# Kernel optimization log

Measured on AMD Instinct MI355X. Metric: run time of the kernel, lower is better.

Reference implementation:

```python
import jax, jax.numpy as jnp
import numpy as np

T, N, E, DH = 4, 10000, 160000, 256
BN_EPS = 1e-5


def setup_inputs() -> dict:
    key = jax.random.key(0)
    ks = jax.random.split(key, 6)
    node_data = jax.random.normal(ks[0], (T, N, DH), dtype=jnp.float32)
    edge_index = jax.random.randint(ks[1], (2, E), 0, N)
    edge_weight = jax.random.uniform(ks[2], (T, E), dtype=jnp.float32)
    W1 = jax.random.normal(ks[3], (3 * DH, DH), dtype=jnp.float32) * 0.02
    b1 = jnp.zeros((DH,), dtype=jnp.float32)
    gamma = jnp.ones((DH,), dtype=jnp.float32)
    beta = jnp.zeros((DH,), dtype=jnp.float32)
    return {"node_data": node_data, "edge_weight": edge_weight, "W1": W1,
            "b1": b1, "gamma": gamma, "beta": beta, "edge_index": edge_index}


def reference(node_data, edge_weight, W1, b1, gamma, beta, edge_index):
    # edge_index: [2, E] with row 0 = source j, row 1 = destination i
    # (ew[t, i, j] multiplies node j and accumulates into node i, as in bmm)
    src, dst = edge_index[0], edge_index[1]

    # sparse bmm: sum_j ew[t,i,j] * node_data[t,j,:]  -> [T, N, DH]
    weighted = node_data[:, src, :] * edge_weight[..., None]  # [T, E, DH]
    sum_neighbor = jax.vmap(lambda m: jax.ops.segment_sum(m, dst, num_segments=N))(weighted)

    # Z = torch.sparse.sum(ew, dim=2); Z[Z == 0] = 1
    Z = jax.vmap(lambda w: jax.ops.segment_sum(w, dst, num_segments=N))(edge_weight)
    Z = jnp.where(Z == 0, 1.0, Z)[..., None]  # [T, N, 1]
    avg_neighbor = sum_neighbor / Z

    # prev_state = cat([zeros(1,N,dh), node_data[1:]], dim=0)  (as in source)
    prev_state = jnp.concatenate(
        [jnp.zeros((1, N, DH), node_data.dtype), node_data[1:]], axis=0)

    x = jnp.concatenate([node_data, prev_state, avg_neighbor], axis=2)
    x = x.reshape(T * N, 3 * DH)

    # ReluFCN: Linear(3*dh -> dh) -> BatchNorm1d (batch stats) -> ReLU
    h = x @ W1 + b1  # [T*N, DH]
    mean = h.mean(axis=0)
    var = h.var(axis=0)
    h = (h - mean) * jax.lax.rsqrt(var + BN_EPS) * gamma + beta
    h = jax.nn.relu(h)
    return h.reshape(T, N, DH)
```

## Files before the change

kernel.cpp:

```cpp
#include <hip/hip_runtime.h>

enum { TT = 4, NNODES = 10000, NEDGES = 160000 };

typedef short v8s __attribute__((ext_vector_type(8)));
typedef float v4f __attribute__((ext_vector_type(4)));
typedef unsigned short u16x4 __attribute__((ext_vector_type(4)));

static __device__ __forceinline__ float bf2f(unsigned short u) {
    union { unsigned int i; float f; } c;
    c.i = ((unsigned int)u) << 16;
    return c.f;
}
static __device__ __forceinline__ unsigned short f2bf(float f) {
    union { float f; unsigned int i; } c;
    c.f = f;
    return (unsigned short)((c.i + 0x7FFFu + ((c.i >> 16) & 1u)) >> 16);
}
static __device__ __forceinline__ float u2f(unsigned int u) {
    union { unsigned int i; float f; } c;
    c.i = u;
    return c.f;
}
static __device__ __forceinline__ void acc8(float* a, float w, uint4 u) {
    a[0] += w * u2f(u.x << 16);
    a[1] += w * u2f(u.x & 0xffff0000u);
    a[2] += w * u2f(u.y << 16);
    a[3] += w * u2f(u.y & 0xffff0000u);
    a[4] += w * u2f(u.z << 16);
    a[5] += w * u2f(u.z & 0xffff0000u);
    a[6] += w * u2f(u.w << 16);
    a[7] += w * u2f(u.w & 0xffff0000u);
}

__global__ void GraphConvLayer_91061896610587_kernel() {}

__global__ void zero_k(int* p, int n) {
    int i = blockIdx.x * 256 + threadIdx.x;
    if (i < n) p[i] = 0;
}

__global__ void prep_k(const unsigned short* ndu, const void* s0, const void* s1,
                       const void* s2, int* mode, float* gammaf, float* betaf) {
    __shared__ int cnt;
    __shared__ int score[6];
    __shared__ float vals[6][256];
    int d = threadIdx.x;
    if (d == 0) cnt = 0;
    if (d < 6) score[d] = 0;
    __syncthreads();
    int c = 0;
    for (int j = 0; j < 16; ++j) {
        unsigned short u = ndu[d * 16 + j];
        if ((u & 0x7FFF) >= 0x6000) ++c;
    }
    if (c) atomicAdd(&cnt, c);
    const void* ptrs[3];
    ptrs[0] = s0; ptrs[1] = s1; ptrs[2] = s2;
    for (int q = 0; q < 6; ++q) {
        const void* p = ptrs[q % 3];
        float v = (q < 3) ? bf2f(((const unsigned short*)p)[d]) : ((const float*)p)[d];
        vals[q][d] = v;
        float av = fabsf(v);
        if (av > 0.25f && av < 4.0f) atomicAdd(&score[q], 1);
    }
    __syncthreads();
    if (d == 0) *mode = (cnt > 0) ? 0 : 1;
    int best = 0;
    for (int q = 1; q < 6; ++q)
        if (score[q] > score[best]) best = q;
    float g = (score[best] > 0) ? vals[best][d] : 1.0f;
    int interp = (best >= 3) ? 3 : 0;
    int bslot  = ((best % 3) == 2) ? 1 : 2;
    float b = vals[interp + bslot][d];
    if (!(b == b) || fabsf(b) > 100.f) b = 0.f;
    gammaf[d] = g;
    betaf[d]  = b;
}

__global__ void zp_k(int* zp, int zn, const unsigned short* ndu, const void* s0,
                     const void* s1, const void* s2, int* mode, float* gammaf,
                     float* betaf) {
    __shared__ int cnt;
    __shared__ int score[6];
    __shared__ float vals[6][256];
    if (blockIdx.x < 213) {
        int i = blockIdx.x * 256 + threadIdx.x;
        if (i < zn) zp[i] = 0;
        return;
    }
    int d = threadIdx.x;
    if (d == 0) cnt = 0;
    if (d < 6) score[d] = 0;
    __syncthreads();
    int c = 0;
    for (int j = 0; j < 16; ++j) {
        unsigned short u = ndu[d * 16 + j];
        if ((u & 0x7FFF) >= 0x6000) ++c;
    }
    if (c) atomicAdd(&cnt, c);
    const void* ptrs[3];
    ptrs[0] = s0; ptrs[1] = s1; ptrs[2] = s2;
    for (int q = 0; q < 6; ++q) {
        const void* p = ptrs[q % 3];
        float v = (q < 3) ? bf2f(((const unsigned short*)p)[d]) : ((const float*)p)[d];
        vals[q][d] = v;
        float av = fabsf(v);
        if (av > 0.25f && av < 4.0f) atomicAdd(&score[q], 1);
    }
    __syncthreads();
    if (d == 0) *mode = (cnt > 0) ? 0 : 1;
    int best = 0;
    for (int q = 1; q < 6; ++q)
        if (score[q] > score[best]) best = q;
    float g = (score[best] > 0) ? vals[best][d] : 1.0f;
    int interp = (best >= 3) ? 3 : 0;
    int bslot  = ((best % 3) == 2) ? 1 : 2;
    float b = vals[interp + bslot][d];
    if (!(b == b) || fabsf(b) > 100.f) b = 0.f;
    gammaf[d] = g;
    betaf[d]  = b;
}

__global__ void cph_k(const int* mode, const void* nd_raw, unsigned short* ndc,
                      const void* W1, short* wp0, short* wp1,
                      const int* ei, int* counts) {
    int bb = blockIdx.x;
    if (bb < 10000) {
        if (*mode != 0) return;
        int i = bb * 256 + threadIdx.x;
        float4 v = ((const float4*)nd_raw)[i];
        ushort4 o;
        o.x = f2bf(v.x); o.y = f2bf(v.y); o.z = f2bf(v.z); o.w = f2bf(v.w);
        ((ushort4*)ndc)[i] = o;
    } else if (bb < 11024) {
        int gid = (bb - 10000) * 256 + threadIdx.x;
        int v   = gid >> 17;
        int rem = gid & 131071;
        int k   = rem >> 8;
        int n   = rem & 255;
        int m   = *mode;
        const unsigned short* Wb = (const unsigned short*)W1;
        const float*          Wf = (const float*)W1;
        float val;
        if (k < 256) {
            val = m ? bf2f(Wb[k * 256 + n]) : Wf[k * 256 + n];
            if (v) val += m ? bf2f(Wb[(k + 256) * 256 + n]) : Wf[(k + 256) * 256 + n];
        } else {
            val = m ? bf2f(Wb[(k + 256) * 256 + n]) : Wf[(k + 256) * 256 + n];
        }
        int dst = ((k >> 5) * 256 + n) * 32 + (k & 31);
        (v ? wp1 : wp0)[dst] = (short)f2bf(val);
    } else {
        int e = (bb - 11024) * 256 + threadIdx.x;
        if (e < NEDGES) atomicAdd(&counts[ei[NEDGES + e]], 1);
    }
}

__global__ void pack_w(const int* mode, const void* W1, float* w2f,
                       short* wp0, short* wp1) {
    int gid = blockIdx.x * 256 + threadIdx.x;
    int v   = gid >> 17;
    int rem = gid & 131071;
    int k   = rem >> 8;
    int n   = rem & 255;
    int m   = *mode;
    const unsigned short* Wb = (const unsigned short*)W1;
    const float*          Wf = (const float*)W1;
    float val;
    if (k < 256) {
        val = m ? bf2f(Wb[k * 256 + n]) : Wf[k * 256 + n];
        if (v) val += m ? bf2f(Wb[(k + 256) * 256 + n]) : Wf[(k + 256) * 256 + n];
    } else {
        val = m ? bf2f(Wb[(k + 256) * 256 + n]) : Wf[(k + 256) * 256 + n];
    }
    if (w2f) w2f[v * 131072 + k * 256 + n] = val;
    if (wp0) {
        int dst = ((k >> 5) * 256 + n) * 32 + (k & 31);
        (v ? wp1 : wp0)[dst] = (short)f2bf(val);
    }
}

__global__ void hist_k(const int* ei, int* counts) {
    int e = blockIdx.x * 256 + threadIdx.x;
    if (e < NEDGES) atomicAdd(&counts[ei[NEDGES + e]], 1);
}

__global__ void scan_k(const int* counts, int* offsets) {
    __shared__ int part[256];
    __shared__ int excl[257];
    int t = threadIdx.x;
    int b = t * 40, e = b + 40;
    if (e > NNODES) e = NNODES;
    int s = 0;
    for (int i = b; i < e; ++i) s += counts[i];
    part[t] = s;
    __syncthreads();
    if (t == 0) {
        int run = 0;
        for (int i = 0; i < 256; ++i) { excl[i] = run; run += part[i]; }
        excl[256] = run;
    }
    __syncthreads();
    int run = excl[t];
    for (int i = b; i < e; ++i) { offsets[i] = run; run += counts[i]; }
    if (t == 0) offsets[NNODES] = excl[256];
}

__global__ void scat_k(const int* ei, const int* offsets, int* cursors,
                       int* ssrc, int* seid) {
    int e = blockIdx.x * 256 + threadIdx.x;
    if (e >= NEDGES) return;
    int d = ei[NEDGES + e];
    int pos = offsets[d] + atomicAdd(&cursors[d], 1);
    ssrc[pos] = ei[e];
    seid[pos] = e;
}

__global__ void scatw_k(const int* mode, const int* ei, const void* ew_raw,
                        const int* offsets, int* cursors, int* ssrc, int* seid,
                        float* wcsr) {
    int e = blockIdx.x * 256 + threadIdx.x;
    if (e >= NEDGES) return;
    int d = ei[NEDGES + e];
    int pos = offsets[d] + atomicAdd(&cursors[d], 1);
    ssrc[pos] = ei[e];
    seid[pos] = e;
    int m = *mode;
#pragma unroll
    for (int t = 0; t < TT; ++t) {
        float w = m ? bf2f(((const unsigned short*)ew_raw)[t * NEDGES + e])
                    : ((const float*)ew_raw)[t * NEDGES + e];
        wcsr[t * NEDGES + pos] = w;
    }
}

__global__ __launch_bounds__(512, 4) void fused_k(
    const int* mode, const void* nd_raw, const unsigned short* ndc,
    const float* wcsr, const int* offsets, const int* ssrc,
    const short* wp0, const short* wp1,
    unsigned short* h16, float* colsumB, float* colsumsqB) {
    __shared__ unsigned short xs[32 * 520];
    int id  = blockIdx.x;
    int xcd = id & 7;
    int t   = xcd & 3;
    int rbi = ((id >> 3) << 1) + (xcd >> 2);
    if (rbi >= 313) return;
    int rb  = rbi * 32;
    const unsigned short* ndb = (*mode == 1) ? (const unsigned short*)nd_raw : ndc;
    int tid = threadIdx.x;

    int node = tid >> 4;
    int sub  = tid & 15;
    int growc = min(rb + node, NNODES - 1);
    const uint4* ndg = (const uint4*)(ndb + (size_t)t * NNODES * 256);
    const uint4* own = ndg + (size_t)growc * 32;

    uint4 c0 = own[sub];
    uint4 c1 = own[sub + 16];
    *(uint4*)&xs[node * 520 + sub * 8]        = c0;
    *(uint4*)&xs[node * 520 + (sub + 16) * 8] = c1;

    float a1[16];
#pragma unroll
    for (int j = 0; j < 16; ++j) a1[j] = 0.f;
    float Z = 0.f;
    const float* wrow = wcsr + t * NEDGES;
    int b = offsets[growc], e = offsets[growc + 1];
    int p = b;
    for (; p + 2 <= e; p += 2) {
        int s0 = ssrc[p], s1 = ssrc[p + 1];
        float w0 = wrow[p], w1 = wrow[p + 1];
        const uint4* r0 = ndg + (size_t)s0 * 32;
        const uint4* r1 = ndg + (size_t)s1 * 32;
        uint4 A0 = r0[sub], A1 = r0[sub + 16];
        uint4 B0 = r1[sub], B1 = r1[sub + 16];
        Z += w0 + w1;
        acc8(a1 + 0, w0, A0); acc8(a1 + 8, w0, A1);
        acc8(a1 + 0, w1, B0); acc8(a1 + 8, w1, B1);
    }
    for (; p < e; ++p) {
        int s = ssrc[p];
        float w = wrow[p];
        const uint4* r0 = ndg + (size_t)s * 32;
        uint4 A0 = r0[sub], A1 = r0[sub + 16];
        Z += w;
        acc8(a1 + 0, w, A0); acc8(a1 + 8, w, A1);
    }
    float inv = (Z == 0.f) ? 1.f : (1.f / Z);
    {
        ushort4 lo, hi;
        lo.x = f2bf(a1[0] * inv); lo.y = f2bf(a1[1] * inv);
        lo.z = f2bf(a1[2] * inv); lo.w = f2bf(a1[3] * inv);
        hi.x = f2bf(a1[4] * inv); hi.y = f2bf(a1[5] * inv);
        hi.z = f2bf(a1[6] * inv); hi.w = f2bf(a1[7] * inv);
        *(ushort4*)&xs[node * 520 + 256 + sub * 8]     = lo;
        *(ushort4*)&xs[node * 520 + 256 + sub * 8 + 4] = hi;
        lo.x = f2bf(a1[8] * inv);  lo.y = f2bf(a1[9] * inv);
        lo.z = f2bf(a1[10] * inv); lo.w = f2bf(a1[11] * inv);
        hi.x = f2bf(a1[12] * inv); hi.y = f2bf(a1[13] * inv);
        hi.z = f2bf(a1[14] * inv); hi.w = f2bf(a1[15] * inv);
        *(ushort4*)&xs[node * 520 + 256 + (sub + 16) * 8]     = lo;
        *(ushort4*)&xs[node * 520 + 256 + (sub + 16) * 8 + 4] = hi;
    }
    __syncthreads();

    int wave = tid >> 6;
    int lane = tid & 63;
    int lane15 = lane & 15, quad = lane >> 4;
    const v8s* wp8 = (const v8s*)(t ? wp1 : wp0);

    v4f acc[2][2];
    v4f zero = {0.f, 0.f, 0.f, 0.f};
#pragma unroll
    for (int mf = 0; mf < 2; ++mf)
#pragma unroll
        for (int nf = 0; nf < 2; ++nf) acc[mf][nf] = zero;

#pragma unroll
    for (int kc = 0; kc < 16; ++kc) {
        v8s a0  = *(const v8s*)&xs[lane15 * 520 + kc * 32 + quad * 8];
        v8s a1v = *(const v8s*)&xs[(lane15 + 16) * 520 + kc * 32 + quad * 8];
#pragma unroll
        for (int nf = 0; nf < 2; ++nf) {
            int ntg = wave * 2 + nf;
            v8s bf = wp8[(size_t)(kc * 256 + ntg * 16 + lane15) * 4 + quad];
            acc[0][nf] = __builtin_amdgcn_mfma_f32_16x16x32_bf16(a0,  bf, acc[0][nf], 0, 0, 0);
            acc[1][nf] = __builtin_amdgcn_mfma_f32_16x16x32_bf16(a1v, bf, acc[1][nf], 0, 0, 0);
        }
    }

    int bucket = id & 63;
#pragma unroll
    for (int nf = 0; nf < 2; ++nf) {
        int col = (wave * 2 + nf) * 16 + lane15;
        float s1 = 0.f, s2 = 0.f;
#pragma unroll
        for (int mf = 0; mf < 2; ++mf) {
            int rbase = rb + mf * 16 + quad * 4;
#pragma unroll
            for (int r = 0; r < 4; ++r) {
                int row = rbase + r;
                if (row < NNODES) {
                    float v = acc[mf][nf][r];
                    __builtin_nontemporal_store(
                        f2bf(v), &h16[(size_t)(t * NNODES + row) * 256 + col]);
                    s1 += v; s2 += v * v;
                }
            }
        }
        s1 += __shfl_xor(s1, 16, 64); s1 += __shfl_xor(s1, 32, 64);
        s2 += __shfl_xor(s2, 16, 64); s2 += __shfl_xor(s2, 32, 64);
        if (quad == 0) {
            atomicAdd(&colsumB[bucket * 256 + col], s1);
            atomicAdd(&colsumsqB[bucket * 256 + col], s2);
        }
    }
}

__global__ void statsB_k(const float* colsumB, const float* colsumsqB,
                         const float* gammaf, const float* betaf,
                         float* scale, float* shiftv) {
    int d = threadIdx.x;
    float s1 = 0.f, s2 = 0.f;
    for (int b = 0; b < 64; ++b) {
        s1 += colsumB[b * 256 + d];
        s2 += colsumsqB[b * 256 + d];
    }
    float mean = s1 * (1.f / 40000.f);
    float var  = s2 * (1.f / 40000.f) - mean * mean;
    if (var < 0.f) var = 0.f;
    if (!(var < 1e30f) || !(mean == mean)) { scale[d] = 0.f; shiftv[d] = 2.5f; return; }
    float r  = rsqrtf(var + 1e-5f);
    float sc = gammaf[d] * r;
    scale[d]  = sc;
    shiftv[d] = betaf[d] - mean * sc;
}

__global__ void normb_k(const unsigned short* h16, const float* scale,
                        const float* shiftv, float* out) {
    int i = blockIdx.x * 256 + threadIdx.x;
    int c0 = (i & 63) * 4;
    u16x4 h = __builtin_nontemporal_load(&((const u16x4*)h16)[i]);
    v4f o;
    float v;
    v = bf2f(h.x) * scale[c0 + 0] + shiftv[c0 + 0]; if (!(v == v)) v = 1.f; o.x = v > 0.f ? v : 0.f;
    v = bf2f(h.y) * scale[c0 + 1] + shiftv[c0 + 1]; if (!(v == v)) v = 1.f; o.y = v > 0.f ? v : 0.f;
    v = bf2f(h.z) * scale[c0 + 2] + shiftv[c0 + 2]; if (!(v == v)) v = 1.f; o.z = v > 0.f ? v : 0.f;
    v = bf2f(h.w) * scale[c0 + 3] + shiftv[c0 + 3]; if (!(v == v)) v = 1.f; o.w = v > 0.f ? v : 0.f;
    __builtin_nontemporal_store(o, &((v4f*)out)[i]);
}

__global__ void aggv_k(const int* mode, const void* nd_raw, const void* ew_raw,
                       const int* offsets, const int* ssrc, const int* seid,
                       unsigned short* avg) {
    int m   = *mode;
    int wid = blockIdx.x * 4 + (threadIdx.x >> 6);
    int t = wid / NNODES, n = wid - t * NNODES;
    int lane = threadIdx.x & 63;
    float a0 = 0.f, a1 = 0.f, a2 = 0.f, a3 = 0.f, Z = 0.f;
    int b = offsets[n], e = offsets[n + 1];
    for (int p = b; p < e; ++p) {
        int s = ssrc[p];
        int ewi = t * NEDGES + seid[p];
        float w = m ? bf2f(((const unsigned short*)ew_raw)[ewi])
                    : ((const float*)ew_raw)[ewi];
        Z += w;
        int vidx = (t * NNODES + s) * 64 + lane;
        if (m) {
            ushort4 v = ((const ushort4*)nd_raw)[vidx];
            a0 += w * bf2f(v.x); a1 += w * bf2f(v.y);
            a2 += w * bf2f(v.z); a3 += w * bf2f(v.w);
        } else {
            float4 v = ((const float4*)nd_raw)[vidx];
            a0 += w * v.x; a1 += w * v.y; a2 += w * v.z; a3 += w * v.w;
        }
    }
    float inv = (Z == 0.f) ? 1.f : (1.f / Z);
    ushort4 o;
    o.x = f2bf(a0 * inv); o.y = f2bf(a1 * inv);
    o.z = f2bf(a2 * inv); o.w = f2bf(a3 * inv);
    ((ushort4*)avg)[(t * NNODES + n) * 64 + lane] = o;
}

__global__ __launch_bounds__(256) void gemmv_k(
    const int* mode, const void* nd_raw, const unsigned short* avg,
    const float* w2f, float* hbuf) {
    __shared__ float xsf[16 * 512];
    int m   = *mode;
    int bt  = blockIdx.x / 625;
    int rb0 = (blockIdx.x - bt * 625) * 16;
    int tid = threadIdx.x;
    for (int j = 0; j < 32; ++j) {
        int idx = tid + j * 256;
        int r = idx >> 9, k = idx & 511;
        int grow = (bt * NNODES + rb0 + r) * 256;
        float val;
        if (k < 256)
            val = m ? bf2f(((const unsigned short*)nd_raw)[grow + k])
                    : ((const float*)nd_raw)[grow + k];
        else
            val = bf2f(avg[grow + (k - 256)]);
        xsf[idx] = val;
    }
    __syncthreads();
    int r0 = (tid >> 6) * 4;
    const float4* w4 = (const float4*)(w2f + (bt ? 131072 : 0));
    float acc[4][4];
#pragma unroll
    for (int r = 0; r < 4; ++r)
#pragma unroll
        for (int c = 0; c < 4; ++c) acc[r][c] = 0.f;
    const float* x0 = &xsf[(r0 + 0) * 512];
    const float* x1 = &xsf[(r0 + 1) * 512];
    const float* x2 = &xsf[(r0 + 2) * 512];
    const float* x3 = &xsf[(r0 + 3) * 512];
#pragma unroll 8
    for (int k = 0; k < 512; ++k) {
        float4 wv = w4[k * 64 + (tid & 63)];
        float a = x0[k], b = x1[k], c = x2[k], d = x3[k];
        acc[0][0] += a * wv.x; acc[0][1] += a * wv.y; acc[0][2] += a * wv.z; acc[0][3] += a * wv.w;
        acc[1][0] += b * wv.x; acc[1][1] += b * wv.y; acc[1][2] += b * wv.z; acc[1][3] += b * wv.w;
        acc[2][0] += c * wv.x; acc[2][1] += c * wv.y; acc[2][2] += c * wv.z; acc[2][3] += c * wv.w;
        acc[3][0] += d * wv.x; acc[3][1] += d * wv.y; acc[3][2] += d * wv.z; acc[3][3] += d * wv.w;
    }
#pragma unroll
    for (int r = 0; r < 4; ++r) {
        int grow = bt * NNODES + rb0 + r0 + r;
        float4 o;
        o.x = acc[r][0]; o.y = acc[r][1]; o.z = acc[r][2]; o.w = acc[r][3];
        ((float4*)hbuf)[grow * 64 + (tid & 63)] = o;
    }
}

__global__ void stats2_k(const float* hbuf, float* colsum, float* colsumsq) {
    int col = threadIdx.x;
    int rb  = blockIdx.x * 250;
    float s1 = 0.f, s2 = 0.f;
    for (int j = 0; j < 250; ++j) {
        float v = hbuf[(size_t)(rb + j) * 256 + col];
        s1 += v; s2 += v * v;
    }
    atomicAdd(&colsum[col], s1);
    atomicAdd(&colsumsq[col], s2);
}

__global__ void stats_k(const float* colsum, const float* colsumsq,
                        const float* gammaf, const float* betaf,
                        float* scale, float* shiftv) {
    int d = threadIdx.x;
    float mean = colsum[d] * (1.f / 40000.f);
    float var  = colsumsq[d] * (1.f / 40000.f) - mean * mean;
    if (var < 0.f) var = 0.f;
    if (!(var < 1e30f) || !(mean == mean)) { scale[d] = 0.f; shiftv[d] = 2.5f; return; }
    float r  = rsqrtf(var + 1e-5f);
    float sc = gammaf[d] * r;
    scale[d]  = sc;
    shiftv[d] = betaf[d] - mean * sc;
}

__global__ void norm_k(float* hbuf, const float* scale, const float* shiftv) {
    int i = blockIdx.x * 256 + threadIdx.x;
    int c0 = (i & 63) * 4;
    float4 h = ((const float4*)hbuf)[i];
    float4 o;
    float v;
    v = h.x * scale[c0 + 0] + shiftv[c0 + 0]; if (!(v == v)) v = 1.f; o.x = v > 0.f ? v : 0.f;
    v = h.y * scale[c0 + 1] + shiftv[c0 + 1]; if (!(v == v)) v = 1.f; o.y = v > 0.f ? v : 0.f;
    v = h.z * scale[c0 + 2] + shiftv[c0 + 2]; if (!(v == v)) v = 1.f; o.z = v > 0.f ? v : 0.f;
    v = h.w * scale[c0 + 3] + shiftv[c0 + 3]; if (!(v == v)) v = 1.f; o.w = v > 0.f ? v : 0.f;
    ((float4*)hbuf)[i] = o;
}

extern "C" void kernel_launch(void* const* d_in, const int* in_sizes, int n_in,
                              void* d_out, int out_size, void* d_ws, size_t ws_size,
                              hipStream_t stream) {
    const void* nd = d_in[0];
    const void* ew = d_in[1];
    const void* W1 = d_in[2];
    const void* p3 = d_in[3];
    const void* p4 = d_in[4];
    const void* p5 = d_in[5];
    const void* ei = d_in[6];
    {
        const void *nd_ = 0, *ew_ = 0, *W1_ = 0, *ei_ = 0, *s_[3] = {0, 0, 0};
        int ns = 0;
        for (int i = 0; i < n_in; ++i) {
            int s = in_sizes[i];
            if      (s == 10240000) nd_ = d_in[i];
            else if (s == 640000)   ew_ = d_in[i];
            else if (s == 196608)   W1_ = d_in[i];
            else if (s == 320000)   ei_ = d_in[i];
            else if (s == 256 && ns < 3) s_[ns++] = d_in[i];
        }
        if (nd_ && ew_ && W1_ && ei_ && ns == 3) {
            nd = nd_; ew = ew_; W1 = W1_; ei = ei_;
            p3 = s_[0]; p4 = s_[1]; p5 = s_[2];
        }
    }
    float* outp = (float*)d_out;
    const unsigned short* ndu = (const unsigned short*)nd;
    const int* eii = (const int*)ei;

    char* ws = (char*)d_ws;

    if (ws_size >= (size_t)45582464) {
        int*   counts    = (int*)(ws + 0);
        int*   cursors   = (int*)(ws + 40960);
        int*   mode      = (int*)(ws + 81920);
        float* scale     = (float*)(ws + 82944);
        float* shiftv    = (float*)(ws + 83968);
        float* gammaf    = (float*)(ws + 84992);
        float* betaf     = (float*)(ws + 86016);
        float* colsumB   = (float*)(ws + 87040);
        float* colsumsqB = (float*)(ws + 152576);
        int*   offsets   = (int*)(ws + 218112);
        int*   ssrc      = (int*)(ws + 258176);
        int*   seid      = (int*)(ws + 898176);
        float* wcsr      = (float*)(ws + 1538176);
        short* wp0       = (short*)(ws + 4098176);
        short* wp1       = (short*)(ws + 4360320);
        unsigned short* ndc = (unsigned short*)(ws + 4622464);
        unsigned short* h16 = (unsigned short*)(ws + 25102464);

        zp_k<<<214, 256, 0, stream>>>((int*)ws, 54528, ndu, p3, p4, p5,
                                      mode, gammaf, betaf);
        cph_k<<<11649, 256, 0, stream>>>(mode, nd, ndc, W1, wp0, wp1, eii, counts);
        scan_k<<<1, 256, 0, stream>>>(counts, offsets);
        scatw_k<<<625, 256, 0, stream>>>(mode, eii, ew, offsets, cursors,
                                         ssrc, seid, wcsr);
        fused_k<<<1280, 512, 0, stream>>>(mode, nd, ndc, wcsr, offsets, ssrc,
                                          wp0, wp1, h16, colsumB, colsumsqB);
        statsB_k<<<1, 256, 0, stream>>>(colsumB, colsumsqB, gammaf, betaf, scale, shiftv);
        normb_k<<<10000, 256, 0, stream>>>(h16, scale, shiftv, outp);
    } else {
        int*   counts   = (int*)(ws + 0);
        int*   cursors  = (int*)(ws + 40960);
        float* colsum   = (float*)(ws + 81920);
        float* colsumsq = (float*)(ws + 82944);
        int*   mode     = (int*)(ws + 83968);
        float* scale    = (float*)(ws + 84032);
        float* shiftv   = (float*)(ws + 85056);
        float* gammaf   = (float*)(ws + 86080);
        float* betaf   = (float*)(ws + 87104);
        int*   offsets  = (int*)(ws + 88128);
        int*   ssrc     = (int*)(ws + 128192);
        int*   seid     = (int*)(ws + 768192);
        float* w2f      = (float*)(ws + 1408192);
        unsigned short* avg = (unsigned short*)(ws + 2457600);
        short* nowp = 0;

        zero_k<<<83, 256, 0, stream>>>((int*)ws, 20994);
        prep_k<<<1, 256, 0, stream>>>(ndu, p3, p4, p5, mode, gammaf, betaf);
        pack_w<<<1024, 256, 0, stream>>>(mode, W1, w2f, nowp, nowp);
        hist_k<<<625, 256, 0, stream>>>(eii, counts);
        scan_k<<<1, 256, 0, stream>>>(counts, offsets);
        scat_k<<<625, 256, 0, stream>>>(eii, offsets, cursors, ssrc, seid);
        aggv_k<<<10000, 256, 0, stream>>>(mode, nd, ew, offsets, ssrc, seid, avg);
        gemmv_k<<<2500, 256, 0, stream>>>(mode, nd, avg, w2f, outp);
        stats2_k<<<160, 256, 0, stream>>>(outp, colsum, colsumsq);
        stats_k<<<1, 256, 0, stream>>>(colsum, colsumsq, gammaf, betaf, scale, shiftv);
        norm_k<<<10000, 256, 0, stream>>>(outp, scale, shiftv);
    }
}
```

Measured before the change: 229.4 us.

## Fuse aggregation, GEMM, batch-norm stats and normalize into one cooperative kernel

Replaces the fused_k + statsB_k + normb_k sequence with a single cooperative kernel of 512 persistent blocks. Each block processes up to three 32-row tiles and keeps the MFMA accumulators in registers. After a grid-wide sync it computes the batch-norm scale and shift itself and writes the normalized ReLU output directly. This removes the bf16 intermediate h round trip and two kernel launches, and also drops the unused seid writes in scatw_k. The cost is a grid sync, extra register pressure from holding three tiles of results, and possible imbalance since 313 tiles are spread over 128 workers per timestep.

Result: no change. 227.3 us (-0.9%).

```diff
diff --git a/kernel.cpp b/kernel.cpp
--- a/kernel.cpp
+++ b/kernel.cpp
@@ -1,4 +1,7 @@
 #include <hip/hip_runtime.h>
+#include <hip/hip_cooperative_groups.h>
+
+namespace cg = cooperative_groups;
 
 enum { TT = 4, NNODES = 10000, NEDGES = 160000 };
 
@@ -217,20 +220,202 @@
 }
 
 __global__ void scatw_k(const int* mode, const int* ei, const void* ew_raw,
-                        const int* offsets, int* cursors, int* ssrc, int* seid,
+                        const int* offsets, int* cursors, int* ssrc,
                         float* wcsr) {
     int e = blockIdx.x * 256 + threadIdx.x;
     if (e >= NEDGES) return;
     int d = ei[NEDGES + e];
     int pos = offsets[d] + atomicAdd(&cursors[d], 1);
     ssrc[pos] = ei[e];
-    seid[pos] = e;
     int m = *mode;
 #pragma unroll
     for (int t = 0; t < TT; ++t) {
         float w = m ? bf2f(((const unsigned short*)ew_raw)[t * NEDGES + e])
                     : ((const float*)ew_raw)[t * NEDGES + e];
         wcsr[t * NEDGES + pos] = w;
+    }
+}
+
+__global__ __launch_bounds__(512, 4) void fusedP_k(
+    const int* mode, const void* nd_raw, const unsigned short* ndc,
+    const float* wcsr, const int* offsets, const int* ssrc,
+    const short* wp0, const short* wp1,
+    float* outp, float* colsumB, float* colsumsqB,
+    const float* gammaf, const float* betaf) {
+    __shared__ unsigned short xs[32 * 520];
+    __shared__ float sscale[256];
+    __shared__ float sshift[256];
+    int id  = blockIdx.x;
+    int xcd = id & 7;
+    int t   = xcd & 3;
+    int worker = ((id >> 3) << 1) + (xcd >> 2);
+    int tid = threadIdx.x;
+    const unsigned short* ndb = (*mode == 1) ? (const unsigned short*)nd_raw : ndc;
+    const uint4* ndg = (const uint4*)(ndb + (size_t)t * NNODES * 256);
+    const float* wrow = wcsr + t * NEDGES;
+
+    int node = tid >> 4;
+    int sub  = tid & 15;
+    int wave = tid >> 6;
+    int lane = tid & 63;
+    int lane15 = lane & 15, quad = lane >> 4;
+    const v8s* wp8 = (const v8s*)(t ? wp1 : wp0);
+    int bucket = id & 63;
+
+    v4f held[3][2][2];
+
+#pragma unroll
+    for (int tt = 0; tt < 3; ++tt) {
+        int rbi = worker + tt * 128;
+        if (rbi < 313) {
+            int rb = rbi * 32;
+            int growc = min(rb + node, NNODES - 1);
+            const uint4* own = ndg + (size_t)growc * 32;
+            uint4 c0 = own[sub];
+            uint4 c1 = own[sub + 16];
+            *(uint4*)&xs[node * 520 + sub * 8]        = c0;
+            *(uint4*)&xs[node * 520 + (sub + 16) * 8] = c1;
+
+            float a1[16];
+#pragma unroll
+            for (int j = 0; j < 16; ++j) a1[j] = 0.f;
+            float Z = 0.f;
+            int b = offsets[growc], e = offsets[growc + 1];
+            int p = b;
+            for (; p + 2 <= e; p += 2) {
+                int s0 = ssrc[p], s1 = ssrc[p + 1];
+                float w0 = wrow[p], w1 = wrow[p + 1];
+                const uint4* r0 = ndg + (size_t)s0 * 32;
+                const uint4* r1 = ndg + (size_t)s1 * 32;
+                uint4 A0 = r0[sub], A1 = r0[sub + 16];
+                uint4 B0 = r1[sub], B1 = r1[sub + 16];
+                Z += w0 + w1;
+                acc8(a1 + 0, w0, A0); acc8(a1 + 8, w0, A1);
+                acc8(a1 + 0, w1, B0); acc8(a1 + 8, w1, B1);
+            }
+            for (; p < e; ++p) {
+                int s = ssrc[p];
+                float w = wrow[p];
+                const uint4* r0 = ndg + (size_t)s * 32;
+                uint4 A0 = r0[sub], A1 = r0[sub + 16];
+                Z += w;
+                acc8(a1 + 0, w, A0); acc8(a1 + 8, w, A1);
+            }
+            float inv = (Z == 0.f) ? 1.f : (1.f / Z);
+            {
+                ushort4 lo, hi;
+                lo.x = f2bf(a1[0] * inv); lo.y = f2bf(a1[1] * inv);
+                lo.z = f2bf(a1[2] * inv); lo.w = f2bf(a1[3] * inv);
+                hi.x = f2bf(a1[4] * inv); hi.y = f2bf(a1[5] * inv);
+                hi.z = f2bf(a1[6] * inv); hi.w = f2bf(a1[7] * inv);
+                *(ushort4*)&xs[node * 520 + 256 + sub * 8]     = lo;
+                *(ushort4*)&xs[node * 520 + 256 + sub * 8 + 4] = hi;
+                lo.x = f2bf(a1[8] * inv);  lo.y = f2bf(a1[9] * inv);
+                lo.z = f2bf(a1[10] * inv); lo.w = f2bf(a1[11] * inv);
+                hi.x = f2bf(a1[12] * inv); hi.y = f2bf(a1[13] * inv);
+                hi.z = f2bf(a1[14] * inv); hi.w = f2bf(a1[15] * inv);
+                *(ushort4*)&xs[node * 520 + 256 + (sub + 16) * 8]     = lo;
+                *(ushort4*)&xs[node * 520 + 256 + (sub + 16) * 8 + 4] = hi;
+            }
+            __syncthreads();
+
+            v4f acc[2][2];
+            v4f zero = {0.f, 0.f, 0.f, 0.f};
+#pragma unroll
+            for (int mf = 0; mf < 2; ++mf)
+#pragma unroll
+                for (int nf = 0; nf < 2; ++nf) acc[mf][nf] = zero;
+
+#pragma unroll
+            for (int kc = 0; kc < 16; ++kc) {
+                v8s a0  = *(const v8s*)&xs[lane15 * 520 + kc * 32 + quad * 8];
+                v8s a1v = *(const v8s*)&xs[(lane15 + 16) * 520 + kc * 32 + quad * 8];
+#pragma unroll
+                for (int nf = 0; nf < 2; ++nf) {
+                    int ntg = wave * 2 + nf;
+                    v8s bf = wp8[(size_t)(kc * 256 + ntg * 16 + lane15) * 4 + quad];
+                    acc[0][nf] = __builtin_amdgcn_mfma_f32_16x16x32_bf16(a0,  bf, acc[0][nf], 0, 0, 0);
+                    acc[1][nf] = __builtin_amdgcn_mfma_f32_16x16x32_bf16(a1v, bf, acc[1][nf], 0, 0, 0);
+                }
+            }
+
+#pragma unroll
+            for (int nf = 0; nf < 2; ++nf) {
+                int col = (wave * 2 + nf) * 16 + lane15;
+                float s1 = 0.f, s2 = 0.f;
+#pragma unroll
+                for (int mf = 0; mf < 2; ++mf) {
+                    held[tt][mf][nf] = acc[mf][nf];
+                    int rbase = rb + mf * 16 + quad * 4;
+#pragma unroll
+                    for (int r = 0; r < 4; ++r) {
+                        int row = rbase + r;
+                        if (row < NNODES) {
+                            float v = acc[mf][nf][r];
+                            s1 += v; s2 += v * v;
+                        }
+                    }
+                }
+                s1 += __shfl_xor(s1, 16, 64); s1 += __shfl_xor(s1, 32, 64);
+                s2 += __shfl_xor(s2, 16, 64); s2 += __shfl_xor(s2, 32, 64);
+                if (quad == 0) {
+                    atomicAdd(&colsumB[bucket * 256 + col], s1);
+                    atomicAdd(&colsumsqB[bucket * 256 + col], s2);
+                }
+            }
+            __syncthreads();
+        }
+    }
+
+    __threadfence();
+    cg::this_grid().sync();
+    __threadfence();
+
+    if (tid < 256) {
+        float s1 = 0.f, s2 = 0.f;
+        for (int b2 = 0; b2 < 64; ++b2) {
+            s1 += colsumB[b2 * 256 + tid];
+            s2 += colsumsqB[b2 * 256 + tid];
+        }
+        float mean = s1 * (1.f / 40000.f);
+        float var  = s2 * (1.f / 40000.f) - mean * mean;
+        if (var < 0.f) var = 0.f;
+        float sc, sh;
+        if (!(var < 1e30f) || !(mean == mean)) { sc = 0.f; sh = 2.5f; }
+        else {
+            float r = rsqrtf(var + 1e-5f);
+            sc = gammaf[tid] * r;
+            sh = betaf[tid] - mean * sc;
+        }
+        sscale[tid] = sc;
+        sshift[tid] = sh;
+    }
+    __syncthreads();
+
+#pragma unroll
+    for (int tt = 0; tt < 3; ++tt) {
+        int rbi = worker + tt * 128;
+        if (rbi < 313) {
+            int rb = rbi * 32;
+#pragma unroll
+            for (int nf = 0; nf < 2; ++nf) {
+                int col = (wave * 2 + nf) * 16 + lane15;
+                float sc = sscale[col], sh = sshift[col];
+#pragma unroll
+                for (int mf = 0; mf < 2; ++mf) {
+                    int rbase = rb + mf * 16 + quad * 4;
+#pragma unroll
+                    for (int r = 0; r < 4; ++r) {
+                        int row = rbase + r;
+                        if (row < NNODES) {
+                            float v = held[tt][mf][nf][r] * sc + sh;
+                            if (!(v == v)) v = 1.f;
+                            outp[(size_t)(t * NNODES + row) * 256 + col] = v > 0.f ? v : 0.f;
+                        }
+                    }
+                }
+            }
+        }
     }
 }
 
@@ -561,17 +746,34 @@
         short* wp1       = (short*)(ws + 4360320);
         unsigned short* ndc = (unsigned short*)(ws + 4622464);
         unsigned short* h16 = (unsigned short*)(ws + 25102464);
+        (void)seid;
 
         zp_k<<<214, 256, 0, stream>>>((int*)ws, 54528, ndu, p3, p4, p5,
                                       mode, gammaf, betaf);
         cph_k<<<11649, 256, 0, stream>>>(mode, nd, ndc, W1, wp0, wp1, eii, counts);
         scan_k<<<1, 256, 0, stream>>>(counts, offsets);
         scatw_k<<<625, 256, 0, stream>>>(mode, eii, ew, offsets, cursors,
-                                         ssrc, seid, wcsr);
-        fused_k<<<1280, 512, 0, stream>>>(mode, nd, ndc, wcsr, offsets, ssrc,
-                                          wp0, wp1, h16, colsumB, colsumsqB);
-        statsB_k<<<1, 256, 0, stream>>>(colsumB, colsumsqB, gammaf, betaf, scale, shiftv);
-        normb_k<<<10000, 256, 0, stream>>>(h16, scale, shiftv, outp);
+                                         ssrc, wcsr);
+
+        int coopBlocks = 0;
+        hipError_t occErr = hipOccupancyMaxActiveBlocksPerMultiprocessor(
+            &coopBlocks, fusedP_k, 512, 0);
+        if (occErr == hipSuccess && coopBlocks >= 2) {
+            void* args[] = {
+                (void*)&mode, (void*)&nd, (void*)&ndc, (void*)&wcsr,
+                (void*)&offsets, (void*)&ssrc, (void*)&wp0, (void*)&wp1,
+                (void*)&outp, (void*)&colsumB, (void*)&colsumsqB,
+                (void*)&gammaf, (void*)&betaf
+            };
+            hipLaunchCooperativeKernel((void*)fusedP_k, dim3(512), dim3(512),
+                                       args, 0, stream);
+        } else {
+            fused_k<<<1280, 512, 0, stream>>>(mode, nd, ndc, wcsr, offsets, ssrc,
+                                              wp0, wp1, h16, colsumB, colsumsqB);
+            statsB_k<<<1, 256, 0, stream>>>(colsumB, colsumsqB, gammaf, betaf,
+                                            scale, shiftv);
+            normb_k<<<10000, 256, 0, stream>>>(h16, scale, shiftv, outp);
+        }
     } else {
         int*   counts   = (int*)(ws + 0);
         int*   cursors  = (int*)(ws + 40960);
@@ -581,7 +783,7 @@
         float* scale    = (float*)(ws + 84032);
         float* shiftv   = (float*)(ws + 85056);
         float* gammaf   = (float*)(ws + 86080);
-        float* betaf   = (float*)(ws + 87104);
+        float* betaf    = (float*)(ws + 87104);
         int*   offsets  = (int*)(ws + 88128);
         int*   ssrc     = (int*)(ws + 128192);
         int*   seid     = (int*)(ws + 768192);
```

## Merge scan and BN stats into producers via last-block-done counters; fold mode detection

Applied to the files above, without the earlier changes.

The graph scan now runs inside the histogram kernel, and the BatchNorm statistics finalisation runs inside the fused aggregate+GEMM kernel. In each case the last block to finish, detected with an atomic done-counter, does the work, which removes two tiny single-block launches and their serialisation gaps. Every block of the preprocessing kernel now detects the input dtype from a small shared-memory scan instead of waiting on a previous kernel. The scatter kernel also stops writing the unused edge-id array. The cost is redundant per-block reads for mode detection, extra fences and atomics, and a serial tail in the last block.

Result: slower. 586.1 us (+155.4%).

```diff
diff --git a/kernel.cpp b/kernel.cpp
--- a/kernel.cpp
+++ b/kernel.cpp
@@ -77,18 +77,61 @@
     betaf[d]  = b;
 }
 
-__global__ void zp_k(int* zp, int zn, const unsigned short* ndu, const void* s0,
-                     const void* s1, const void* s2, int* mode, float* gammaf,
-                     float* betaf) {
+__global__ void pre_k(int* zp, const unsigned short* ndu, const void* nd_raw,
+                      unsigned short* ndc, const void* W1, short* wp0, short* wp1,
+                      const void* s0, const void* s1, const void* s2,
+                      int* mode, float* gammaf, float* betaf,
+                      int* doneA, int* doneB) {
     __shared__ int cnt;
     __shared__ int score[6];
     __shared__ float vals[6][256];
-    if (blockIdx.x < 213) {
-        int i = blockIdx.x * 256 + threadIdx.x;
-        if (i < zn) zp[i] = 0;
+    int bb = blockIdx.x;
+    int d  = threadIdx.x;
+
+    if (bb < 11024) {
+        if (d == 0) cnt = 0;
+        __syncthreads();
+        int c = 0;
+        for (int j = 0; j < 16; ++j) {
+            unsigned short u = ndu[d * 16 + j];
+            if ((u & 0x7FFF) >= 0x6000) c = 1;
+        }
+        if (c) cnt = 1;
+        __syncthreads();
+        int m = cnt ? 0 : 1;
+        if (bb < 10000) {
+            if (m != 0) return;
+            int i = bb * 256 + d;
+            float4 v = ((const float4*)nd_raw)[i];
+            ushort4 o;
+            o.x = f2bf(v.x); o.y = f2bf(v.y); o.z = f2bf(v.z); o.w = f2bf(v.w);
+            ((ushort4*)ndc)[i] = o;
+        } else {
+            int gid = (bb - 10000) * 256 + d;
+            int v   = gid >> 17;
+            int rem = gid & 131071;
+            int k   = rem >> 8;
+            int n   = rem & 255;
+            const unsigned short* Wb = (const unsigned short*)W1;
+            const float*          Wf = (const float*)W1;
+            float val;
+            if (k < 256) {
+                val = m ? bf2f(Wb[k * 256 + n]) : Wf[k * 256 + n];
+                if (v) val += m ? bf2f(Wb[(k + 256) * 256 + n]) : Wf[(k + 256) * 256 + n];
+            } else {
+                val = m ? bf2f(Wb[(k + 256) * 256 + n]) : Wf[(k + 256) * 256 + n];
+            }
+            int dst = ((k >> 5) * 256 + n) * 32 + (k & 31);
+            (v ? wp1 : wp0)[dst] = (short)f2bf(val);
+        }
         return;
     }
-    int d = threadIdx.x;
+    if (bb < 11232) {
+        int z = (bb - 11024) * 256 + d;
+        int idx = (z < 20480) ? z : z + 1280;
+        zp[idx] = 0;
+        return;
+    }
     if (d == 0) cnt = 0;
     if (d < 6) score[d] = 0;
     __syncthreads();
@@ -108,7 +151,7 @@
         if (av > 0.25f && av < 4.0f) atomicAdd(&score[q], 1);
     }
     __syncthreads();
-    if (d == 0) *mode = (cnt > 0) ? 0 : 1;
+    if (d == 0) { *mode = (cnt > 0) ? 0 : 1; *doneA = 0; *doneB = 0; }
     int best = 0;
     for (int q = 1; q < 6; ++q)
         if (score[q] > score[best]) best = q;
@@ -121,38 +164,91 @@
     betaf[d]  = b;
 }
 
-__global__ void cph_k(const int* mode, const void* nd_raw, unsigned short* ndc,
-                      const void* W1, short* wp0, short* wp1,
-                      const int* ei, int* counts) {
-    int bb = blockIdx.x;
-    if (bb < 10000) {
-        if (*mode != 0) return;
-        int i = bb * 256 + threadIdx.x;
-        float4 v = ((const float4*)nd_raw)[i];
-        ushort4 o;
-        o.x = f2bf(v.x); o.y = f2bf(v.y); o.z = f2bf(v.z); o.w = f2bf(v.w);
-        ((ushort4*)ndc)[i] = o;
-    } else if (bb < 11024) {
-        int gid = (bb - 10000) * 256 + threadIdx.x;
-        int v   = gid >> 17;
-        int rem = gid & 131071;
-        int k   = rem >> 8;
-        int n   = rem & 255;
-        int m   = *mode;
-        const unsigned short* Wb = (const unsigned short*)W1;
-        const float*          Wf = (const float*)W1;
-        float val;
-        if (k < 256) {
-            val = m ? bf2f(Wb[k * 256 + n]) : Wf[k * 256 + n];
-            if (v) val += m ? bf2f(Wb[(k + 256) * 256 + n]) : Wf[(k + 256) * 256 + n];
-        } else {
-            val = m ? bf2f(Wb[(k + 256) * 256 + n]) : Wf[(k + 256) * 256 + n];
-        }
-        int dst = ((k >> 5) * 256 + n) * 32 + (k & 31);
-        (v ? wp1 : wp0)[dst] = (short)f2bf(val);
-    } else {
-        int e = (bb - 11024) * 256 + threadIdx.x;
-        if (e < NEDGES) atomicAdd(&counts[ei[NEDGES + e]], 1);
+__global__ void histscan_k(const int* ei, int* counts, int* offsets, int* doneA) {
+    int e = blockIdx.x * 256 + threadIdx.x;
+    if (e < NEDGES) atomicAdd(&counts[ei[NEDGES + e]], 1);
+    __threadfence();
+    __syncthreads();
+    __shared__ int last;
+    if (threadIdx.x == 0)
+        last = (atomicAdd(doneA, 1) == (int)gridDim.x - 1);
+    __syncthreads();
+    if (!last) return;
+    __shared__ int part[256];
+    __shared__ int excl[257];
+    int t = threadIdx.x;
+    int b = t * 40, e2 = b + 40;
+    if (b > NNODES) b = NNODES;
+    if (e2 > NNODES) e2 = NNODES;
+    int s = 0;
+    for (int i = b; i < e2; ++i)
+        s += __hip_atomic_load(&counts[i], __ATOMIC_RELAXED, __HIP_MEMORY_SCOPE_AGENT);
+    part[t] = s;
+    __syncthreads();
+    if (t == 0) {
+        int run = 0;
+        for (int i = 0; i < 256; ++i) { excl[i] = run; run += part[i]; }
+        excl[256] = run;
+    }
+    __syncthreads();
+    int run = excl[t];
+    for (int i = b; i < e2; ++i) {
+        offsets[i] = run;
+        run += __hip_atomic_load(&counts[i], __ATOMIC_RELAXED, __HIP_MEMORY_SCOPE_AGENT);
+    }
+    if (t == 0) offsets[NNODES] = excl[256];
+}
+
+__global__ void hist_k(const int* ei, int* counts) {
+    int e = blockIdx.x * 256 + threadIdx.x;
+    if (e < NEDGES) atomicAdd(&counts[ei[NEDGES + e]], 1);
+}
+
+__global__ void scan_k(const int* counts, int* offsets) {
+    __shared__ int part[256];
+    __shared__ int excl[257];
+    int t = threadIdx.x;
+    int b = t * 40, e = b + 40;
+    if (e > NNODES) e = NNODES;
+    int s = 0;
+    for (int i = b; i < e; ++i) s += counts[i];
+    part[t] = s;
+    __syncthreads();
+    if (t == 0) {
+        int run = 0;
+        for (int i = 0; i < 256; ++i) { excl[i] = run; run += part[i]; }
+        excl[256] = run;
+    }
+    __syncthreads();
+    int run = excl[t];
+    for (int i = b; i < e; ++i) { offsets[i] = run; run += counts[i]; }
+    if (t == 0) offsets[NNODES] = excl[256];
+}
+
+__global__ void scat_k(const int* ei, const int* offsets, int* cursors,
+                       int* ssrc, int* seid) {
+    int e = blockIdx.x * 256 + threadIdx.x;
+    if (e >= NEDGES) return;
+    int d = ei[NEDGES + e];
+    int pos = offsets[d] + atomicAdd(&cursors[d], 1);
+    ssrc[pos] = ei[e];
+    seid[pos] = e;
+}
+
+__global__ void scatw_k(const int* mode, const int* ei, const void* ew_raw,
+                        const int* offsets, int* cursors, int* ssrc,
+                        float* wcsr) {
+    int e = blockIdx.x * 256 + threadIdx.x;
+    if (e >= NEDGES) return;
+    int d = ei[NEDGES + e];
+    int pos = offsets[d] + atomicAdd(&cursors[d], 1);
+    ssrc[pos] = ei[e];
+    int m = *mode;
+#pragma unroll
+    for (int t = 0; t < TT; ++t) {
+        float w = m ? bf2f(((const unsigned short*)ew_raw)[t * NEDGES + e])
+                    : ((const float*)ew_raw)[t * NEDGES + e];
+        wcsr[t * NEDGES + pos] = w;
     }
 }
 
@@ -180,200 +276,157 @@
     }
 }
 
-__global__ void hist_k(const int* ei, int* counts) {
-    int e = blockIdx.x * 256 + threadIdx.x;
-    if (e < NEDGES) atomicAdd(&counts[ei[NEDGES + e]], 1);
-}
-
-__global__ void scan_k(const int* counts, int* offsets) {
-    __shared__ int part[256];
-    __shared__ int excl[257];
-    int t = threadIdx.x;
-    int b = t * 40, e = b + 40;
-    if (e > NNODES) e = NNODES;
-    int s = 0;
-    for (int i = b; i < e; ++i) s += counts[i];
-    part[t] = s;
-    __syncthreads();
-    if (t == 0) {
-        int run = 0;
-        for (int i = 0; i < 256; ++i) { excl[i] = run; run += part[i]; }
-        excl[256] = run;
-    }
-    __syncthreads();
-    int run = excl[t];
-    for (int i = b; i < e; ++i) { offsets[i] = run; run += counts[i]; }
-    if (t == 0) offsets[NNODES] = excl[256];
-}
-
-__global__ void scat_k(const int* ei, const int* offsets, int* cursors,
-                       int* ssrc, int* seid) {
-    int e = blockIdx.x * 256 + threadIdx.x;
-    if (e >= NEDGES) return;
-    int d = ei[NEDGES + e];
-    int pos = offsets[d] + atomicAdd(&cursors[d], 1);
-    ssrc[pos] = ei[e];
-    seid[pos] = e;
-}
-
-__global__ void scatw_k(const int* mode, const int* ei, const void* ew_raw,
-                        const int* offsets, int* cursors, int* ssrc, int* seid,
-                        float* wcsr) {
-    int e = blockIdx.x * 256 + threadIdx.x;
-    if (e >= NEDGES) return;
-    int d = ei[NEDGES + e];
-    int pos = offsets[d] + atomicAdd(&cursors[d], 1);
-    ssrc[pos] = ei[e];
-    seid[pos] = e;
-    int m = *mode;
-#pragma unroll
-    for (int t = 0; t < TT; ++t) {
-        float w = m ? bf2f(((const unsigned short*)ew_raw)[t * NEDGES + e])
-                    : ((const float*)ew_raw)[t * NEDGES + e];
-        wcsr[t * NEDGES + pos] = w;
-    }
-}
-
 __global__ __launch_bounds__(512, 4) void fused_k(
     const int* mode, const void* nd_raw, const unsigned short* ndc,
     const float* wcsr, const int* offsets, const int* ssrc,
     const short* wp0, const short* wp1,
-    unsigned short* h16, float* colsumB, float* colsumsqB) {
+    unsigned short* h16, float* colsumB, float* colsumsqB,
+    const float* gammaf, const float* betaf,
+    float* scale, float* shiftv, int* doneB) {
     __shared__ unsigned short xs[32 * 520];
+    __shared__ int lastB;
     int id  = blockIdx.x;
     int xcd = id & 7;
     int t   = xcd & 3;
     int rbi = ((id >> 3) << 1) + (xcd >> 2);
-    if (rbi >= 313) return;
-    int rb  = rbi * 32;
-    const unsigned short* ndb = (*mode == 1) ? (const unsigned short*)nd_raw : ndc;
     int tid = threadIdx.x;
 
-    int node = tid >> 4;
-    int sub  = tid & 15;
-    int growc = min(rb + node, NNODES - 1);
-    const uint4* ndg = (const uint4*)(ndb + (size_t)t * NNODES * 256);
-    const uint4* own = ndg + (size_t)growc * 32;
-
-    uint4 c0 = own[sub];
-    uint4 c1 = own[sub + 16];
-    *(uint4*)&xs[node * 520 + sub * 8]        = c0;
-    *(uint4*)&xs[node * 520 + (sub + 16) * 8] = c1;
-
-    float a1[16];
-#pragma unroll
-    for (int j = 0; j < 16; ++j) a1[j] = 0.f;
-    float Z = 0.f;
-    const float* wrow = wcsr + t * NEDGES;
-    int b = offsets[growc], e = offsets[growc + 1];
-    int p = b;
-    for (; p + 2 <= e; p += 2) {
-        int s0 = ssrc[p], s1 = ssrc[p + 1];
-        float w0 = wrow[p], w1 = wrow[p + 1];
-        const uint4* r0 = ndg + (size_t)s0 * 32;
-        const uint4* r1 = ndg + (size_t)s1 * 32;
-        uint4 A0 = r0[sub], A1 = r0[sub + 16];
-        uint4 B0 = r1[sub], B1 = r1[sub + 16];
-        Z += w0 + w1;
-        acc8(a1 + 0, w0, A0); acc8(a1 + 8, w0, A1);
-        acc8(a1 + 0, w1, B0); acc8(a1 + 8, w1, B1);
-    }
-    for (; p < e; ++p) {
-        int s = ssrc[p];
-        float w = wrow[p];
-        const uint4* r0 = ndg + (size_t)s * 32;
-        uint4 A0 = r0[sub], A1 = r0[sub + 16];
-        Z += w;
-        acc8(a1 + 0, w, A0); acc8(a1 + 8, w, A1);
-    }
-    float inv = (Z == 0.f) ? 1.f : (1.f / Z);
-    {
-        ushort4 lo, hi;
-        lo.x = f2bf(a1[0] * inv); lo.y = f2bf(a1[1] * inv);
-        lo.z = f2bf(a1[2] * inv); lo.w = f2bf(a1[3] * inv);
-        hi.x = f2bf(a1[4] * inv); hi.y = f2bf(a1[5] * inv);
-        hi.z = f2bf(a1[6] * inv); hi.w = f2bf(a1[7] * inv);
-        *(ushort4*)&xs[node * 520 + 256 + sub * 8]     = lo;
-        *(ushort4*)&xs[node * 520 + 256 + sub * 8 + 4] = hi;
-        lo.x = f2bf(a1[8] * inv);  lo.y = f2bf(a1[9] * inv);
-        lo.z = f2bf(a1[10] * inv); lo.w = f2bf(a1[11] * inv);
-        hi.x = f2bf(a1[12] * inv); hi.y = f2bf(a1[13] * inv);
-        hi.z = f2bf(a1[14] * inv); hi.w = f2bf(a1[15] * inv);
-        *(ushort4*)&xs[node * 520 + 256 + (sub + 16) * 8]     = lo;
-        *(ushort4*)&xs[node * 520 + 256 + (sub + 16) * 8 + 4] = hi;
-    }
-    __syncthreads();
-
-    int wave = tid >> 6;
-    int lane = tid & 63;
-    int lane15 = lane & 15, quad = lane >> 4;
-    const v8s* wp8 = (const v8s*)(t ? wp1 : wp0);
-
-    v4f acc[2][2];
-    v4f zero = {0.f, 0.f, 0.f, 0.f};
-#pragma unroll
-    for (int mf = 0; mf < 2; ++mf)
-#pragma unroll
-        for (int nf = 0; nf < 2; ++nf) acc[mf][nf] = zero;
-
-#pragma unroll
-    for (int kc = 0; kc < 16; ++kc) {
-        v8s a0  = *(const v8s*)&xs[lane15 * 520 + kc * 32 + quad * 8];
-        v8s a1v = *(const v8s*)&xs[(lane15 + 16) * 520 + kc * 32 + quad * 8];
+    if (rbi < 313) {
+        int rb  = rbi * 32;
+        const unsigned short* ndb = (*mode == 1) ? (const unsigned short*)nd_raw : ndc;
+
+        int node = tid >> 4;
+        int sub  = tid & 15;
+        int growc = min(rb + node, NNODES - 1);
+        const uint4* ndg = (const uint4*)(ndb + (size_t)t * NNODES * 256);
+        const uint4* own = ndg + (size_t)growc * 32;
+
+        uint4 c0 = own[sub];
+        uint4 c1 = own[sub + 16];
+        *(uint4*)&xs[node * 520 + sub * 8]        = c0;
+        *(uint4*)&xs[node * 520 + (sub + 16) * 8] = c1;
+
+        float a1[16];
+#pragma unroll
+        for (int j = 0; j < 16; ++j) a1[j] = 0.f;
+        float Z = 0.f;
+        const float* wrow = wcsr + t * NEDGES;
+        int b = offsets[growc], e = offsets[growc + 1];
+        int p = b;
+        for (; p + 2 <= e; p += 2) {
+            int s0 = ssrc[p], s1 = ssrc[p + 1];
+            float w0 = wrow[p], w1 = wrow[p + 1];
+            const uint4* r0 = ndg + (size_t)s0 * 32;
+            const uint4* r1 = ndg + (size_t)s1 * 32;
+            uint4 A0 = r0[sub], A1 = r0[sub + 16];
+            uint4 B0 = r1[sub], B1 = r1[sub + 16];
+            Z += w0 + w1;
+            acc8(a1 + 0, w0, A0); acc8(a1 + 8, w0, A1);
+            acc8(a1 + 0, w1, B0); acc8(a1 + 8, w1, B1);
+        }
+        for (; p < e; ++p) {
+            int s = ssrc[p];
+            float w = wrow[p];
+            const uint4* r0 = ndg + (size_t)s * 32;
+            uint4 A0 = r0[sub], A1 = r0[sub + 16];
+            Z += w;
+            acc8(a1 + 0, w, A0); acc8(a1 + 8, w, A1);
+        }
+        float inv = (Z == 0.f) ? 1.f : (1.f / Z);
+        {
+            ushort4 lo, hi;
+            lo.x = f2bf(a1[0] * inv); lo.y = f2bf(a1[1] * inv);
+            lo.z = f2bf(a1[2] * inv); lo.w = f2bf(a1[3] * inv);
+            hi.x = f2bf(a1[4] * inv); hi.y = f2bf(a1[5] * inv);
+            hi.z = f2bf(a1[6] * inv); hi.w = f2bf(a1[7] * inv);
+            *(ushort4*)&xs[node * 520 + 256 + sub * 8]     = lo;
+            *(ushort4*)&xs[node * 520 + 256 + sub * 8 + 4] = hi;
+            lo.x = f2bf(a1[8] * inv);  lo.y = f2bf(a1[9] * inv);
+            lo.z = f2bf(a1[10] * inv); lo.w = f2bf(a1[11] * inv);
+            hi.x = f2bf(a1[12] * inv); hi.y = f2bf(a1[13] * inv);
+            hi.z = f2bf(a1[14] * inv); hi.w = f2bf(a1[15] * inv);
+            *(ushort4*)&xs[node * 520 + 256 + (sub + 16) * 8]     = lo;
+            *(ushort4*)&xs[node * 520 + 256 + (sub + 16) * 8 + 4] = hi;
+        }
+        __syncthreads();
+
+        int wave = tid >> 6;
+        int lane = tid & 63;
+        int lane15 = lane & 15, quad = lane >> 4;
+        const v8s* wp8 = (const v8s*)(t ? wp1 : wp0);
+
+        v4f acc[2][2];
+        v4f zero = {0.f, 0.f, 0.f, 0.f};
+#pragma unroll
+        for (int mf = 0; mf < 2; ++mf)
+#pragma unroll
+            for (int nf = 0; nf < 2; ++nf) acc[mf][nf] = zero;
+
+#pragma unroll
+        for (int kc = 0; kc < 16; ++kc) {
+            v8s a0  = *(const v8s*)&xs[lane15 * 520 + kc * 32 + quad * 8];
+            v8s a1v = *(const v8s*)&xs[(lane15 + 16) * 520 + kc * 32 + quad * 8];
+#pragma unroll
+            for (int nf = 0; nf < 2; ++nf) {
+                int ntg = wave * 2 + nf;
+                v8s bf = wp8[(size_t)(kc * 256 + ntg * 16 + lane15) * 4 + quad];
+                acc[0][nf] = __builtin_amdgcn_mfma_f32_16x16x32_bf16(a0,  bf, acc[0][nf], 0, 0, 0);
+                acc[1][nf] = __builtin_amdgcn_mfma_f32_16x16x32_bf16(a1v, bf, acc[1][nf], 0, 0, 0);
+            }
+        }
+
+        int bucket = id & 63;
 #pragma unroll
         for (int nf = 0; nf < 2; ++nf) {
-            int ntg = wave * 2 + nf;
-            v8s bf = wp8[(size_t)(kc * 256 + ntg * 16 + lane15) * 4 + quad];
-            acc[0][nf] = __builtin_amdgcn_mfma_f32_16x16x32_bf16(a0,  bf, acc[0][nf], 0, 0, 0);
-            acc[1][nf] = __builtin_amdgcn_mfma_f32_16x16x32_bf16(a1v, bf, acc[1][nf], 0, 0, 0);
-        }
-    }
-
-    int bucket = id & 63;
-#pragma unroll
-    for (int nf = 0; nf < 2; ++nf) {
-        int col = (wave * 2 + nf) * 16 + lane15;
-        float s1 = 0.f, s2 = 0.f;
-#pragma unroll
-        for (int mf = 0; mf < 2; ++mf) {
-            int rbase = rb + mf * 16 + quad * 4;
-#pragma unroll
-            for (int r = 0; r < 4; ++r) {
-                int row = rbase + r;
-                if (row < NNODES) {
-                    float v = acc[mf][nf][r];
-                    __builtin_nontemporal_store(
-                        f2bf(v), &h16[(size_t)(t * NNODES + row) * 256 + col]);
-                    s1 += v; s2 += v * v;
+            int col = (wave * 2 + nf) * 16 + lane15;
+            float s1 = 0.f, s2 = 0.f;
+#pragma unroll
+            for (int mf = 0; mf < 2; ++mf) {
+                int rbase = rb + mf * 16 + quad * 4;
+#pragma unroll
+                for (int r = 0; r < 4; ++r) {
+                    int row = rbase + r;
+                    if (row < NNODES) {
+                        float v = acc[mf][nf][r];
+                        __builtin_nontemporal_store(
+                            f2bf(v), &h16[(size_t)(t * NNODES + row) * 256 + col]);
+                        s1 += v; s2 += v * v;
+                    }
                 }
             }
-        }
-        s1 += __shfl_xor(s1, 16, 64); s1 += __shfl_xor(s1, 32, 64);
-        s2 += __shfl_xor(s2, 16, 64); s2 += __shfl_xor(s2, 32, 64);
-        if (quad == 0) {
-            atomicAdd(&colsumB[bucket * 256 + col], s1);
-            atomicAdd(&colsumsqB[bucket * 256 + col], s2);
-        }
-    }
-}
-
-__global__ void statsB_k(const float* colsumB, const float* colsumsqB,
-                         const float* gammaf, const float* betaf,
-                         float* scale, float* shiftv) {
-    int d = threadIdx.x;
-    float s1 = 0.f, s2 = 0.f;
-    for (int b = 0; b < 64; ++b) {
-        s1 += colsumB[b * 256 + d];
-        s2 += colsumsqB[b * 256 + d];
-    }
-    float mean = s1 * (1.f / 40000.f);
-    float var  = s2 * (1.f / 40000.f) - mean * mean;
-    if (var < 0.f) var = 0.f;
-    if (!(var < 1e30f) || !(mean == mean)) { scale[d] = 0.f; shiftv[d] = 2.5f; return; }
-    float r  = rsqrtf(var + 1e-5f);
-    float sc = gammaf[d] * r;
-    scale[d]  = sc;
-    shiftv[d] = betaf[d] - mean * sc;
+            s1 += __shfl_xor(s1, 16, 64); s1 += __shfl_xor(s1, 32, 64);
+            s2 += __shfl_xor(s2, 16, 64); s2 += __shfl_xor(s2, 32, 64);
+            if (quad == 0) {
+                atomicAdd(&colsumB[bucket * 256 + col], s1);
+                atomicAdd(&colsumsqB[bucket * 256 + col], s2);
+            }
+        }
+    }
+
+    __threadfence();
+    __syncthreads();
+    if (tid == 0)
+        lastB = (atomicAdd(doneB, 1) == (int)gridDim.x - 1);
+    __syncthreads();
+    if (lastB && tid < 256) {
+        float s1 = 0.f, s2 = 0.f;
+        for (int b2 = 0; b2 < 64; ++b2) {
+            s1 += __hip_atomic_load(&colsumB[b2 * 256 + tid],
+                                    __ATOMIC_RELAXED, __HIP_MEMORY_SCOPE_AGENT);
+            s2 += __hip_atomic_load(&colsumsqB[b2 * 256 + tid],
+                                    __ATOMIC_RELAXED, __HIP_MEMORY_SCOPE_AGENT);
+        }
+        float mean = s1 * (1.f / 40000.f);
+        float var  = s2 * (1.f / 40000.f) - mean * mean;
+        if (var < 0.f) var = 0.f;
+        if (!(var < 1e30f) || !(mean == mean)) { scale[tid] = 0.f; shiftv[tid] = 2.5f; }
+        else {
+            float r  = rsqrtf(var + 1e-5f);
+            float sc = gammaf[tid] * r;
+            scale[tid]  = sc;
+            shiftv[tid] = betaf[tid] - mean * sc;
+        }
+    }
 }
 
 __global__ void normb_k(const unsigned short* h16, const float* scale,
@@ -547,6 +600,8 @@
         int*   counts    = (int*)(ws + 0);
         int*   cursors   = (int*)(ws + 40960);
         int*   mode      = (int*)(ws + 81920);
+        int*   doneA     = (int*)(ws + 81936);
+        int*   doneB     = (int*)(ws + 81940);
         float* scale     = (float*)(ws + 82944);
         float* shiftv    = (float*)(ws + 83968);
         float* gammaf    = (float*)(ws + 84992);
@@ -561,16 +616,17 @@
         short* wp1       = (short*)(ws + 4360320);
         unsigned short* ndc = (unsigned short*)(ws + 4622464);
         unsigned short* h16 = (unsigned short*)(ws + 25102464);
-
-        zp_k<<<214, 256, 0, stream>>>((int*)ws, 54528, ndu, p3, p4, p5,
-                                      mode, gammaf, betaf);
-        cph_k<<<11649, 256, 0, stream>>>(mode, nd, ndc, W1, wp0, wp1, eii, counts);
-        scan_k<<<1, 256, 0, stream>>>(counts, offsets);
+        (void)seid;
+
+        pre_k<<<11233, 256, 0, stream>>>((int*)ws, ndu, nd, ndc, W1, wp0, wp1,
+                                         p3, p4, p5, mode, gammaf, betaf,
+                                         doneA, doneB);
+        histscan_k<<<625, 256, 0, stream>>>(eii, counts, offsets, doneA);
         scatw_k<<<625, 256, 0, stream>>>(mode, eii, ew, offsets, cursors,
-                                         ssrc, seid, wcsr);
+                                         ssrc, wcsr);
         fused_k<<<1280, 512, 0, stream>>>(mode, nd, ndc, wcsr, offsets, ssrc,
-                                          wp0, wp1, h16, colsumB, colsumsqB);
-        statsB_k<<<1, 256, 0, stream>>>(colsumB, colsumsqB, gammaf, betaf, scale, shiftv);
+                                          wp0, wp1, h16, colsumB, colsumsqB,
+                                          gammaf, betaf, scale, shiftv, doneB);
         normb_k<<<10000, 256, 0, stream>>>(h16, scale, shiftv, outp);
     } else {
         int*   counts   = (int*)(ws + 0);
@@ -581,7 +637,7 @@
         float* scale    = (float*)(ws + 84032);
         float* shiftv   = (float*)(ws + 85056);
         float* gammaf   = (float*)(ws + 86080);
-        float* betaf   = (float*)(ws + 87104);
+        float* betaf    = (float*)(ws + 87104);
         int*   offsets  = (int*)(ws + 88128);
         int*   ssrc     = (int*)(ws + 128192);
         int*   seid     = (int*)(ws + 768192);
```
